# Performance work log

Hardware: AMD Instinct MI355X
Metric: run time of the kernel (lower is better)

The kernel has to match this reference:

```python
import jax, jax.numpy as jnp
import numpy as np

HEADS = 4  # from init_kwargs

def _branch_index(seq_len: int) -> jnp.ndarray:
    # position 0 -> layer_s(0), 1 -> layer_r(1), 2 -> layer_o(2),
    # then alternating layer_a(3)/layer_v(4) starting at position 3.
    tail = jnp.where((jnp.arange(seq_len - 3) % 2) == 0, 3, 4)
    return jnp.concatenate([jnp.array([0, 1, 2], dtype=tail.dtype), tail])


def setup_inputs() -> dict:
    key = jax.random.key(0)
    k1, k2, k3 = jax.random.split(key, 3)
    B, S, H = 128, 513, 256
    x = jax.random.normal(k1, (B, S, H), dtype=jnp.float32)
    # 5 Linear layers, nn.Linear convention: y = x @ W.T + b, W: [out,in]
    W = jax.random.normal(k2, (5, H, H), dtype=jnp.float32) * (1.0 / np.sqrt(H))
    b = jax.random.normal(k3, (5, H), dtype=jnp.float32) * 0.02
    return {"x": x, "W": W, "b": b}


def reference(x, W, b):
    # Original applies each Linear to a position-masked copy of x and sums.
    # Since the 5 masks are disjoint one-hots over positions, the weight term
    # at position t is x[t] @ W[m(t)].T; the bias term is sum of ALL 5 biases
    # (Linear(0) = bias), applied at every position.
    B, S, H = x.shape
    idx = _branch_index(S)            # [S] in {0..4}
    Wsel = W[idx]
    out = jnp.einsum('bsh,sdh->bsd', x, Wsel) + b.sum(axis=0)
    return out.reshape(B, S, HEADS, H // HEADS)
```

## Files before the change

### kernel.cpp

```cpp
#include <hip/hip_runtime.h>
#include <hip/hip_bf16.h>

#define B_ 128
#define S_ 513
#define H_ 256
#define SH_ (S_ * H_)

typedef __attribute__((ext_vector_type(8))) short short8;
typedef __attribute__((ext_vector_type(4))) float f32x4;

static __device__ inline short8 pack8(float4 a, float4 b) {
    union { short8 s; __hip_bfloat162 h[4]; } u;
    u.h[0] = __float22bfloat162_rn(make_float2(a.x, a.y));
    u.h[1] = __float22bfloat162_rn(make_float2(a.z, a.w));
    u.h[2] = __float22bfloat162_rn(make_float2(b.x, b.y));
    u.h[3] = __float22bfloat162_rn(make_float2(b.z, b.w));
    return u.s;
}
static __device__ inline short8 pack8v(f32x4 a, f32x4 b) {
    union { short8 s; __hip_bfloat162 h[4]; } u;
    u.h[0] = __float22bfloat162_rn(make_float2(a[0], a[1]));
    u.h[1] = __float22bfloat162_rn(make_float2(a[2], a[3]));
    u.h[2] = __float22bfloat162_rn(make_float2(b[0], b[1]));
    u.h[3] = __float22bfloat162_rn(make_float2(b[2], b[3]));
    return u.s;
}

__global__ void prep_kernel(const float* __restrict__ W,
                            const float* __restrict__ bias,
                            unsigned short* __restrict__ Wbf,
                            float* __restrict__ bsum) {
    int t = blockIdx.x * 256 + threadIdx.x;
    if (t < 5 * 32 * 256) {
        int m  = t >> 13;
        int r  = t & 8191;
        int d  = r >> 5;
        int kc = r & 31;
        const float* src = W + (((size_t)m * 256 + d) * 256 + kc * 8);
        float4 v0 = *(const float4*)src;
        float4 v1 = *(const float4*)(src + 4);
        *(short8*)(Wbf + ((size_t)(m * 32 + kc) * 256 + d) * 8) = pack8(v0, v1);
    }
    if (t < H_) {
        float s = 0.f;
#pragma unroll
        for (int i = 0; i < 5; ++i) s += bias[i * H_ + t];
        bsum[t] = s;
    }
}

template <int MODE>
__global__ __launch_bounds__(256, 4)
void sel_gemm_kernel(const float* __restrict__ x,
                     const void* __restrict__ Wp,
                     const void* __restrict__ bp,
                     float* __restrict__ out) {
    const int bid = blockIdx.x;
    int m_idx, rmax, rowstride;
    size_t rowbase;
    if (bid < 2048) {
        const int b    = bid >> 4;
        const int sub  = bid & 15;
        const int par  = sub & 1;
        const int tile = sub >> 1;
        const int sbase = (par ? 3 : 4) + tile * 64;
        m_idx     = par ? 3 : 4;
        rowbase   = (size_t)b * S_ + sbase;
        rowstride = 2;
        rmax      = (512 - sbase) >> 1;
        if (rmax > 31) rmax = 31;
    } else {
        const int e  = bid - 2048;
        const int s  = e >> 2;
        const int bq = e & 3;
        m_idx     = s;
        rowbase   = (size_t)(bq * 32) * S_ + s;
        rowstride = S_;
        rmax      = 31;
    }

    __shared__ float As[32 * 256];

    const int t    = threadIdx.x;
    const int lane = t & 63;
    const int w    = t >> 6;
    const int lrow = lane & 15;
    const int quad = lane >> 4;

#pragma unroll
    for (int it = 0; it < 8; ++it) {
        const int r  = it * 4 + w;
        const int rc = r <= rmax ? r : rmax;
        const float* src = x + (rowbase + (size_t)rowstride * rc) * H_
                             + ((lane ^ (r & 7)) << 2);
        __builtin_amdgcn_global_load_lds(
            (const __attribute__((address_space(1))) unsigned int*)src,
            (__attribute__((address_space(3))) unsigned int*)&As[r * 256],
            16, 0, 0);
    }

    f32x4 acc[2][4];
#pragma unroll
    for (int i = 0; i < 2; ++i)
#pragma unroll
        for (int j = 0; j < 4; ++j) {
            f32x4 z = {0.f, 0.f, 0.f, 0.f};
            acc[i][j] = z;
        }

    __syncthreads();

#pragma unroll
    for (int kk = 0; kk < 8; ++kk) {
        short8 wfr[4];
        if (MODE == 0) {
            const unsigned short* Wk =
                (const unsigned short*)Wp +
                ((size_t)(m_idx * 32 + kk * 4 + quad) * 256) * 8;
#pragma unroll
            for (int j = 0; j < 4; ++j)
                wfr[j] = *(const short8*)(Wk + (size_t)(w * 64 + j * 16 + lrow) * 8);
        } else {
            const float* Wb = (const float*)Wp + (size_t)m_idx * H_ * H_;
#pragma unroll
            for (int j = 0; j < 4; ++j) {
                const float* wrow = Wb + (size_t)(w * 64 + j * 16 + lrow) * H_
                                    + kk * 32 + quad * 8;
                float4 v0 = *(const float4*)wrow;
                float4 v1 = *(const float4*)(wrow + 4);
                wfr[j] = pack8(v0, v1);
            }
        }

        short8 xfr[2];
        const int g0 = kk * 8 + quad * 2;
#pragma unroll
        for (int i = 0; i < 2; ++i) {
            const int r = i * 16 + lrow;
            f32x4 f0 = *(const f32x4*)&As[r * 256 + (((g0    ) ^ (r & 7)) << 2)];
            f32x4 f1 = *(const f32x4*)&As[r * 256 + (((g0 + 1) ^ (r & 7)) << 2)];
            xfr[i] = pack8v(f0, f1);
        }

#pragma unroll
        for (int j = 0; j < 4; ++j)
#pragma unroll
            for (int i = 0; i < 2; ++i)
                acc[i][j] = __builtin_amdgcn_mfma_f32_16x16x32_bf16(
                    wfr[j], xfr[i], acc[i][j], 0, 0, 0);
    }

#pragma unroll
    for (int j = 0; j < 4; ++j) {
        const int d0 = w * 64 + j * 16 + quad * 4;
        f32x4 bj;
        if (MODE == 0) {
            bj = *(const f32x4*)((const float*)bp + d0);
        } else {
            const float* bias = (const float*)bp;
#pragma unroll
            for (int r = 0; r < 4; ++r) {
                float sum = 0.f;
#pragma unroll
                for (int i = 0; i < 5; ++i) sum += bias[i * H_ + d0 + r];
                bj[r] = sum;
            }
        }
#pragma unroll
        for (int i = 0; i < 2; ++i) {
            const int r = i * 16 + lrow;
            if (r <= rmax) {
                f32x4 v = acc[i][j] + bj;
                *(f32x4*)(out + (rowbase + (size_t)rowstride * r) * H_ + d0) = v;
            }
        }
    }
}

extern "C" void kernel_launch(void* const* d_in, const int* in_sizes, int n_in,
                              void* d_out, int out_size, void* d_ws, size_t ws_size,
                              hipStream_t stream) {
    const float* x    = (const float*)d_in[0];
    const float* W    = (const float*)d_in[1];
    const float* bias = (const float*)d_in[2];
    float* out = (float*)d_out;

    const size_t w_elems  = (size_t)5 * H_ * H_;
    const size_t ws_need  = w_elems * sizeof(unsigned short) + H_ * sizeof(float);

    const int grid = 2048 + 12;
    if (ws_size >= ws_need) {
        unsigned short* Wbf = (unsigned short*)d_ws;
        float* bsum = (float*)((char*)d_ws + w_elems * sizeof(unsigned short));
        prep_kernel<<<dim3(160), dim3(256), 0, stream>>>(W, bias, Wbf, bsum);
        sel_gemm_kernel<0><<<dim3(grid), dim3(256), 0, stream>>>(
            x, (const void*)Wbf, (const void*)bsum, out);
    } else {
        sel_gemm_kernel<1><<<dim3(grid), dim3(256), 0, stream>>>(
            x, (const void*)W, (const void*)bias, out);
    }
}
```

Before: 132.0 us.

## Use 8-wave blocks and preload all weight fragments before the x tile

Result: no change. 131.1 us (-0.6%).

```diff
diff --git a/kernel.cpp b/kernel.cpp
--- a/kernel.cpp
+++ b/kernel.cpp
@@ -50,60 +50,107 @@
 }
 
 template <int MODE>
-__global__ __launch_bounds__(256, 4)
+__global__ __launch_bounds__(512, 4)
 void sel_gemm_kernel(const float* __restrict__ x,
                      const void* __restrict__ Wp,
                      const void* __restrict__ bp,
                      float* __restrict__ out) {
-    const int bid = blockIdx.x;
-    int m_idx, rmax, rowstride;
-    size_t rowbase;
+    __shared__ float As[32 * 256];
+
+    const int bid  = blockIdx.x;
+    const int t    = threadIdx.x;
+    const int lane = t & 63;
+    const int w8   = t >> 6;
+    const int lrow = lane & 15;
+    const int quad = lane >> 4;
+
+    int m_idx, rmax;
+    size_t xrow0, rstride;
     if (bid < 2048) {
-        const int b    = bid >> 4;
-        const int sub  = bid & 15;
-        const int par  = sub & 1;
-        const int tile = sub >> 1;
-        const int sbase = (par ? 3 : 4) + tile * 64;
-        m_idx     = par ? 3 : 4;
-        rowbase   = (size_t)b * S_ + sbase;
-        rowstride = 2;
-        rmax      = (512 - sbase) >> 1;
+        const int b   = bid >> 4;
+        const int sub = bid & 15;
+        const int par = sub & 1;
+        const int q   = sub >> 1;
+        const int sbase = (par ? 3 : 4) + q * 64;
+        m_idx   = par ? 3 : 4;
+        xrow0   = (size_t)b * S_ + sbase;
+        rstride = 2;
+        rmax    = (512 - sbase) >> 1;
         if (rmax > 31) rmax = 31;
     } else {
         const int e  = bid - 2048;
         const int s  = e >> 2;
         const int bq = e & 3;
-        m_idx     = s;
-        rowbase   = (size_t)(bq * 32) * S_ + s;
-        rowstride = S_;
-        rmax      = 31;
-    }
-
-    __shared__ float As[32 * 256];
-
-    const int t    = threadIdx.x;
-    const int lane = t & 63;
-    const int w    = t >> 6;
-    const int lrow = lane & 15;
-    const int quad = lane >> 4;
-
-#pragma unroll
-    for (int it = 0; it < 8; ++it) {
-        const int r  = it * 4 + w;
-        const int rc = r <= rmax ? r : rmax;
-        const float* src = x + (rowbase + (size_t)rowstride * rc) * H_
-                             + ((lane ^ (r & 7)) << 2);
+        m_idx   = s;
+        xrow0   = (size_t)(bq * 32) * S_ + s;
+        rstride = S_;
+        rmax    = 31;
+    }
+
+    short8 wfr[2][8];
+    if (MODE == 0) {
+        const unsigned short* Wb = (const unsigned short*)Wp;
+#pragma unroll
+        for (int kk = 0; kk < 8; ++kk) {
+            const unsigned short* Wk =
+                Wb + ((size_t)(m_idx * 32 + kk * 4 + quad) * 256) * 8;
+#pragma unroll
+            for (int j = 0; j < 2; ++j)
+                wfr[j][kk] = *(const short8*)(Wk +
+                              (size_t)(w8 * 32 + j * 16 + lrow) * 8);
+        }
+    } else {
+        const float* Wb = (const float*)Wp + (size_t)m_idx * H_ * H_;
+#pragma unroll
+        for (int kk = 0; kk < 8; ++kk)
+#pragma unroll
+            for (int j = 0; j < 2; ++j) {
+                const float* wrow = Wb +
+                    (size_t)(w8 * 32 + j * 16 + lrow) * H_ + kk * 32 + quad * 8;
+                float4 v0 = *(const float4*)wrow;
+                float4 v1 = *(const float4*)(wrow + 4);
+                wfr[j][kk] = pack8(v0, v1);
+            }
+    }
+
+#pragma unroll
+    for (int it = 0; it < 4; ++it) {
+        const int row = w8 * 4 + it;
+        int rg = row <= rmax ? row : rmax;
+        const float* src = x + (xrow0 + rstride * rg) * H_
+                             + ((lane ^ (row & 7)) << 2);
         __builtin_amdgcn_global_load_lds(
             (const __attribute__((address_space(1))) unsigned int*)src,
-            (__attribute__((address_space(3))) unsigned int*)&As[r * 256],
+            (__attribute__((address_space(3))) unsigned int*)&As[row * 256],
             16, 0, 0);
     }
 
-    f32x4 acc[2][4];
+    f32x4 bj[2];
+    if (MODE == 0) {
+        const float* bsum = (const float*)bp;
+#pragma unroll
+        for (int j = 0; j < 2; ++j)
+            bj[j] = *(const f32x4*)(bsum + w8 * 32 + j * 16 + quad * 4);
+    } else {
+        const float* bias = (const float*)bp;
+#pragma unroll
+        for (int j = 0; j < 2; ++j) {
+            const int d0 = w8 * 32 + j * 16 + quad * 4;
+#pragma unroll
+            for (int r = 0; r < 4; ++r) {
+                float sum = 0.f;
+#pragma unroll
+                for (int i = 0; i < 5; ++i) sum += bias[i * H_ + d0 + r];
+                bj[j][r] = sum;
+            }
+        }
+    }
+
+    f32x4 acc[2][2];
 #pragma unroll
     for (int i = 0; i < 2; ++i)
 #pragma unroll
-        for (int j = 0; j < 4; ++j) {
+        for (int j = 0; j < 2; ++j) {
             f32x4 z = {0.f, 0.f, 0.f, 0.f};
             acc[i][j] = z;
         }
@@ -112,26 +159,6 @@
 
 #pragma unroll
     for (int kk = 0; kk < 8; ++kk) {
-        short8 wfr[4];
-        if (MODE == 0) {
-            const unsigned short* Wk =
-                (const unsigned short*)Wp +
-                ((size_t)(m_idx * 32 + kk * 4 + quad) * 256) * 8;
-#pragma unroll
-            for (int j = 0; j < 4; ++j)
-                wfr[j] = *(const short8*)(Wk + (size_t)(w * 64 + j * 16 + lrow) * 8);
-        } else {
-            const float* Wb = (const float*)Wp + (size_t)m_idx * H_ * H_;
-#pragma unroll
-            for (int j = 0; j < 4; ++j) {
-                const float* wrow = Wb + (size_t)(w * 64 + j * 16 + lrow) * H_
-                                    + kk * 32 + quad * 8;
-                float4 v0 = *(const float4*)wrow;
-                float4 v1 = *(const float4*)(wrow + 4);
-                wfr[j] = pack8(v0, v1);
-            }
-        }
-
         short8 xfr[2];
         const int g0 = kk * 8 + quad * 2;
 #pragma unroll
@@ -141,37 +168,23 @@
             f32x4 f1 = *(const f32x4*)&As[r * 256 + (((g0 + 1) ^ (r & 7)) << 2)];
             xfr[i] = pack8v(f0, f1);
         }
-
-#pragma unroll
-        for (int j = 0; j < 4; ++j)
+#pragma unroll
+        for (int j = 0; j < 2; ++j)
 #pragma unroll
             for (int i = 0; i < 2; ++i)
                 acc[i][j] = __builtin_amdgcn_mfma_f32_16x16x32_bf16(
-                    wfr[j], xfr[i], acc[i][j], 0, 0, 0);
-    }
-
-#pragma unroll
-    for (int j = 0; j < 4; ++j) {
-        const int d0 = w * 64 + j * 16 + quad * 4;
-        f32x4 bj;
-        if (MODE == 0) {
-            bj = *(const f32x4*)((const float*)bp + d0);
-        } else {
-            const float* bias = (const float*)bp;
-#pragma unroll
-            for (int r = 0; r < 4; ++r) {
-                float sum = 0.f;
-#pragma unroll
-                for (int i = 0; i < 5; ++i) sum += bias[i * H_ + d0 + r];
-                bj[r] = sum;
-            }
-        }
+                    wfr[j][kk], xfr[i], acc[i][j], 0, 0, 0);
+    }
+
+#pragma unroll
+    for (int j = 0; j < 2; ++j) {
+        const int d0 = w8 * 32 + j * 16 + quad * 4;
 #pragma unroll
         for (int i = 0; i < 2; ++i) {
-            const int r = i * 16 + lrow;
-            if (r <= rmax) {
-                f32x4 v = acc[i][j] + bj;
-                *(f32x4*)(out + (rowbase + (size_t)rowstride * r) * H_ + d0) = v;
+            const int rg = i * 16 + lrow;
+            if (rg <= rmax) {
+                f32x4 v = acc[i][j] + bj[j];
+                *(f32x4*)(out + (xrow0 + rstride * rg) * H_ + d0) = v;
             }
         }
     }
@@ -193,10 +206,10 @@
         unsigned short* Wbf = (unsigned short*)d_ws;
         float* bsum = (float*)((char*)d_ws + w_elems * sizeof(unsigned short));
         prep_kernel<<<dim3(160), dim3(256), 0, stream>>>(W, bias, Wbf, bsum);
-        sel_gemm_kernel<0><<<dim3(grid), dim3(256), 0, stream>>>(
+        sel_gemm_kernel<0><<<dim3(grid), dim3(512), 0, stream>>>(
             x, (const void*)Wbf, (const void*)bsum, out);
     } else {
-        sel_gemm_kernel<1><<<dim3(grid), dim3(256), 0, stream>>>(
+        sel_gemm_kernel<1><<<dim3(grid), dim3(512), 0, stream>>>(
             x, (const void*)W, (const void*)bias, out);
     }
 }
```
